# Optimization experiments

Hardware: AMD Instinct MI355X
Metric: run time of the kernel (lower is better)

Reference implementation:

```python
import jax, jax.numpy as jnp
import numpy as np
from jax import lax

EPS = 1e-5


def _conv3x3(inp, w):
    # NCHW input, OIHW kernel, VALID padding, stride 1 (matches nn.Conv2d(k=3, s=1, p=0))
    return lax.conv_general_dilated(inp, w, (1, 1), 'VALID',
                                    dimension_numbers=('NCHW', 'OIHW', 'NCHW'))


def _bn(h, gamma, beta, mean, var):
    # inference-mode BatchNorm2d
    inv = gamma / jnp.sqrt(var + EPS)
    return h * inv[None, :, None, None] + (beta - mean * inv)[None, :, None, None]


def _xcorr_depthwise(zf, xf):
    # per-sample, per-channel sliding cross-correlation: template zf over search xf
    B, C, Hz, Wz = zf.shape
    _, _, Hx, Wx = xf.shape
    xr = xf.reshape(1, B * C, Hx, Wx)
    kr = zf.reshape(B * C, 1, Hz, Wz)
    out = lax.conv_general_dilated(xr, kr, (1, 1), 'VALID',
                                   feature_group_count=B * C,
                                   dimension_numbers=('NCHW', 'OIHW', 'NCHW'))
    return out.reshape(B, C, out.shape[2], out.shape[3])


def setup_inputs() -> dict:
    key = jax.random.key(0)
    ks = jax.random.split(key, 12)
    B, Cin, Ch = 64, 256, 256
    z = jax.random.normal(ks[0], (B, Cin, 16, 16), dtype=jnp.float32)
    x = jax.random.normal(ks[1], (B, Cin, 32, 32), dtype=jnp.float32)
    # conv weights ~ N(0, 0.01) as in _initialize_weights
    w_z = 0.01 * jax.random.normal(ks[2], (Ch, Cin, 3, 3), dtype=jnp.float32)
    w_x = 0.01 * jax.random.normal(ks[3], (Ch, Cin, 3, 3), dtype=jnp.float32)
    gamma_z = 0.5 + jax.random.uniform(ks[4], (Ch,), dtype=jnp.float32)
    beta_z = 0.1 * jax.random.normal(ks[5], (Ch,), dtype=jnp.float32)
    mean_z = 0.1 * jax.random.normal(ks[6], (Ch,), dtype=jnp.float32)
    var_z = 0.5 + jax.random.uniform(ks[7], (Ch,), dtype=jnp.float32)
    gamma_x = 0.5 + jax.random.uniform(ks[8], (Ch,), dtype=jnp.float32)
    beta_x = 0.1 * jax.random.normal(ks[9], (Ch,), dtype=jnp.float32)
    mean_x = 0.1 * jax.random.normal(ks[10], (Ch,), dtype=jnp.float32)
    var_x = 0.5 + jax.random.uniform(ks[11], (Ch,), dtype=jnp.float32)
    return {'z': z, 'x': x, 'w_z': w_z, 'w_x': w_x,
            'gamma_z': gamma_z, 'beta_z': beta_z, 'mean_z': mean_z, 'var_z': var_z,
            'gamma_x': gamma_x, 'beta_x': beta_x, 'mean_x': mean_x, 'var_x': var_x}


def reference(z, x, w_z, w_x, gamma_z, beta_z, mean_z, var_z,
              gamma_x, beta_x, mean_x, var_x):
    zf = _bn(_conv3x3(z, w_z), gamma_z, beta_z, mean_z, var_z)   # [B,C,14,14]
    xf = _bn(_conv3x3(x, w_x), gamma_x, beta_x, mean_x, var_x)   # [B,C,30,30]
    return _xcorr_depthwise(zf, xf)                               # [B,C,17,17]
```

## Files before the change

kernel.cpp:

```cpp
#include <hip/hip_runtime.h>
#include <cstdint>
#include <cstddef>

typedef _Float16 f16;
typedef _Float16 half4 __attribute__((ext_vector_type(4)));
typedef _Float16 half8 __attribute__((ext_vector_type(8)));
typedef __fp16 fp16x2 __attribute__((ext_vector_type(2)));
typedef float f32x4 __attribute__((ext_vector_type(4)));

#define BN_EPS 1e-5f

#if defined(__has_builtin)
# if __has_builtin(__builtin_amdgcn_fdot2)
#  define HAVE_FDOT2 1
# endif
#endif
#ifndef HAVE_FDOT2
# define HAVE_FDOT2 0
#endif

static constexpr size_t OFF_XB  = 0;
static constexpr size_t OFF_ZB  = 33554432;
static constexpr size_t OFF_WX  = 41943040;
static constexpr size_t OFF_WZ  = 43122688;
static constexpr size_t OFF_BNX = 44302336;
static constexpr size_t OFF_BNZ = 44304384;
static constexpr size_t OFF_XFH = 44306432;
static constexpr size_t OFF_ZFH = 75763712;

__global__ __launch_bounds__(256) void prep_all(
    const float* __restrict__ x, const float* __restrict__ z,
    const float* __restrict__ w_x, const float* __restrict__ w_z,
    const float* __restrict__ gx, const float* __restrict__ bx,
    const float* __restrict__ mx, const float* __restrict__ vx,
    const float* __restrict__ gz, const float* __restrict__ bz,
    const float* __restrict__ mz, const float* __restrict__ vz,
    f16* __restrict__ xb, f16* __restrict__ zb,
    f16* __restrict__ wxA, f16* __restrict__ wzA,
    float* __restrict__ bnx, float* __restrict__ bnz) {
  __shared__ float tile[64][33];
  __shared__ alignas(16) f16 wtile[2304];
  const int bid = blockIdx.x;
  const int tid = threadIdx.x;
  if (bid < 12288) {
    const float* src; f16* dst; int lw, r;
    if (bid < 8192) { src = x; dst = xb; lw = 5; r = bid; }
    else            { src = z; dst = zb; lw = 4; r = bid - 8192; }
    const int W = 1 << lw;
    const int c0 = (r & 3) << 6;
    const int h = (r >> 2) & (W - 1);
    const int b = (r >> 2) >> lw;
    const float* sp = src + ((size_t)((b << 8) + c0) << (2 * lw)) + ((size_t)h << lw);
    const int w4 = W >> 2;
    const int n1 = w4 << 6;
    for (int i = tid; i < n1; i += 256) {
      int cl = i >> (lw - 2), c4 = i & (w4 - 1);
      float4 v = *(const float4*)(sp + ((size_t)cl << (2 * lw)) + (c4 << 2));
      int w0 = c4 << 2;
      tile[cl][w0] = v.x; tile[cl][w0 + 1] = v.y;
      tile[cl][w0 + 2] = v.z; tile[cl][w0 + 3] = v.w;
    }
    __syncthreads();
    f16* dp = dst + ((size_t)((b << lw) + h) << lw << 8) + c0;
    const int n2 = W << 3;
    for (int j = tid; j < n2; j += 256) {
      int w = j >> 3, cl0 = (j & 7) << 3;
      half8 o;
#pragma unroll
      for (int e = 0; e < 8; ++e) o[e] = (f16)tile[cl0 + e][w];
      *(half8*)(dp + (w << 8) + cl0) = o;
    }
  } else if (bid < 12800) {
    int r = bid - 12288;
    const float* src = (r < 256) ? w_x : w_z;
    f16* dst = (r < 256) ? wxA : wzA;
    int cout = r & 255;
    const float* sp = src + (size_t)cout * 2304;
    for (int i = tid; i < 2304; i += 256) {
      int cin = i / 9, khw = i - cin * 9;
      wtile[khw * 256 + cin] = (f16)sp[i];
    }
    __syncthreads();
    for (int c = tid; c < 288; c += 256) {
      int khw = c >> 5, cin0 = (c & 31) << 3;
      *(half8*)(dst + (khw << 16) + (cout << 8) + cin0) =
          *(const half8*)(wtile + khw * 256 + cin0);
    }
  } else {
    int c = tid;
    float iv = gx[c] / sqrtf(vx[c] + BN_EPS);
    bnx[c] = iv;
    bnx[256 + c] = bx[c] - mx[c] * iv;
    float iz = gz[c] / sqrtf(vz[c] + BN_EPS);
    bnz[c] = iz;
    bnz[256 + c] = bz[c] - mz[c] * iz;
  }
}

__device__ __forceinline__ void gl_lds16(const f16* g, f16* l) {
  __builtin_amdgcn_global_load_lds((__attribute__((address_space(1))) void*)g,
                                   (__attribute__((address_space(3))) void*)l, 16, 0, 0);
}

__global__ __launch_bounds__(256, 4) void conv_gemm_u(
    const f16* __restrict__ xb, const f16* __restrict__ zb,
    const f16* __restrict__ wx, const f16* __restrict__ wz,
    const float* __restrict__ bnx, const float* __restrict__ bnz,
    f16* __restrict__ xfh, f16* __restrict__ zfh) {
  __shared__ f16 As[128 * 64];
  __shared__ f16 Bs[128 * 64];
  const int g = blockIdx.x;
  const int pairIdx = ((g >> 4) << 3) | (g & 7);
  const int mblk = (g >> 3) & 1;
  if (pairIdx >= 548) return;
  const f16* inp; const f16* wA; const float* bn; f16* out;
  int nblk, HIN, WIN, WOUT, NPIX, WPAD, OPLANE;
  if (pairIdx < 450) {
    inp = xb; wA = wx; bn = bnx; out = xfh; nblk = pairIdx;
    HIN = 32; WIN = 32; WOUT = 30; NPIX = 900; WPAD = 32; OPLANE = 960;
  } else {
    inp = zb; wA = wz; bn = bnz; out = zfh; nblk = pairIdx - 450;
    HIN = 16; WIN = 16; WOUT = 14; NPIX = 196; WPAD = 16; OPLANE = 224;
  }
  const int tid = threadIdx.x;
  const int wid = tid >> 6, lane = tid & 63;
  const int wm = (wid >> 1) << 6, wn = (wid & 1) << 6;
  const int q = lane >> 4, lm = lane & 15;
  const int sr = lane >> 3, sc = lane & 7;
  const int swz = (sc ^ sr) << 3;
  const int mbase = mblk << 7;

  int arow[4], brow[4];
#pragma unroll
  for (int l = 0; l < 4; ++l) {
    int rr = (wid << 5) + (l << 3) + sr;
    arow[l] = ((mbase + rr) << 8) + swz;
    int n = (nblk << 7) + rr;
    int b = n / NPIX, rem = n - b * NPIX;
    int oh = rem / WOUT, ow = rem - oh * WOUT;
    brow[l] = (((b * HIN + oh) * WIN + ow) << 8) + swz;
  }

  f32x4 acc[4][4] = {};
  const int cA0 = (q ^ (lm & 7)) << 3;

  for (int kt = 0; kt < 36; ++kt) {
    const int cinb = kt / 9;
    const int khw = kt - cinb * 9;
    const int cin0 = cinb << 6;
    const int kh = khw / 3, kw = khw - kh * 3;
    const int wofs = (khw << 16) + cin0;
    const int iofs = ((kh * WIN + kw) << 8) + cin0;
#pragma unroll
    for (int l = 0; l < 4; ++l) {
      const int ldso = ((wid << 5) + (l << 3)) << 6;
      gl_lds16(wA + wofs + arow[l], As + ldso);
      gl_lds16(inp + iofs + brow[l], Bs + ldso);
    }
    __syncthreads();
#pragma unroll
    for (int h = 0; h < 2; ++h) {
      const int co = cA0 ^ (h << 5);
      half8 af[4], bf[4];
#pragma unroll
      for (int f = 0; f < 4; ++f) {
        af[f] = *(const half8*)&As[((wm + (f << 4) + lm) << 6) + co];
        bf[f] = *(const half8*)&Bs[((wn + (f << 4) + lm) << 6) + co];
      }
#pragma unroll
      for (int fm = 0; fm < 4; ++fm)
#pragma unroll
        for (int fn = 0; fn < 4; ++fn)
          acc[fm][fn] =
              __builtin_amdgcn_mfma_f32_16x16x32_f16(af[fm], bf[fn], acc[fm][fn], 0, 0, 0);
    }
    __syncthreads();
  }

#pragma unroll
  for (int fn = 0; fn < 4; ++fn) {
    int n_g = (nblk << 7) + wn + (fn << 4) + lm;
    int b = n_g / NPIX, rem = n_g - b * NPIX;
    int oh = rem / WOUT, ow = rem - oh * WOUT;
    f16* op = out + (size_t)(b << 8) * OPLANE + oh * WPAD + ow;
#pragma unroll
    for (int fm = 0; fm < 4; ++fm) {
      int m0 = mbase + wm + (fm << 4) + (q << 2);
#pragma unroll
      for (int rg = 0; rg < 4; ++rg) {
        int m = m0 + rg;
        op[(size_t)m * OPLANE] = (f16)(acc[fm][fn][rg] * bn[m] + bn[256 + m]);
      }
    }
  }
}

static constexpr int XST = 40;
static constexpr int XCH = 30 * XST;
static constexpr int ZCH = 14 * 16;

__global__ __launch_bounds__(256) void xcorr_dw3(const f16* __restrict__ zfh,
                                                 const f16* __restrict__ xfh,
                                                 float* __restrict__ out) {
  __shared__ f16 xs[3 * XCH];
  __shared__ f16 zs[3 * ZCH];
  const int t = threadIdx.x;
  const int ch0 = blockIdx.x * 3;

  for (int i = t; i < 360; i += 256) {
    int ch = i / 120, rem = i - ch * 120;
    int row = rem >> 2, col = (rem & 3) << 3;
    if (ch0 + ch < 16384)
      *(half8*)(xs + ch * XCH + row * XST + col) =
          *(const half8*)(xfh + (size_t)(ch0 + ch) * 960 + row * 32 + col);
  }
  for (int i = t; i < 84; i += 256) {
    int ch = i / 28, rem = i - ch * 28;
    if (ch0 + ch < 16384)
      *(half8*)(zs + ch * ZCH + rem * 8) =
          *(const half8*)(zfh + (size_t)(ch0 + ch) * 224 + rem * 8);
  }
  __syncthreads();

  int lc = t / 85;
  int r = t - lc * 85;
  const bool ok = (lc < 3) && (ch0 + lc < 16384);
  if (lc > 2) lc = 2;
  const int oy = r / 5, oxq = r - oy * 5, ox0 = oxq * 4;
  const f16* xbp = xs + lc * XCH;
  const f16* zbp = zs + lc * ZCH;

  float acc[4] = {0.f, 0.f, 0.f, 0.f};

#if HAVE_FDOT2
  union X20 { half4 v4[5]; fp16x2 h2[10]; };
  union Z16 { half8 v8[2]; fp16x2 h2[8]; };
#pragma unroll 2
  for (int u = 0; u < 14; ++u) {
    X20 xl;
#pragma unroll
    for (int k = 0; k < 5; ++k)
      xl.v4[k] = *(const half4*)(xbp + (oy + u) * XST + ox0 + (k << 2));
    Z16 zl;
    zl.v8[0] = *(const half8*)(zbp + u * 16);
    zl.v8[1] = *(const half8*)(zbp + u * 16 + 8);
    fp16x2 xo[8];
#pragma unroll
    for (int m = 0; m < 8; ++m) { xo[m][0] = xl.h2[m][1]; xo[m][1] = xl.h2[m + 1][0]; }
#pragma unroll
    for (int k = 0; k < 7; ++k) {
      acc[0] = __builtin_amdgcn_fdot2(zl.h2[k], xl.h2[k],     acc[0], false);
      acc[1] = __builtin_amdgcn_fdot2(zl.h2[k], xo[k],        acc[1], false);
      acc[2] = __builtin_amdgcn_fdot2(zl.h2[k], xl.h2[k + 1], acc[2], false);
      acc[3] = __builtin_amdgcn_fdot2(zl.h2[k], xo[k + 1],    acc[3], false);
    }
  }
#else
#pragma unroll 2
  for (int u = 0; u < 14; ++u) {
    float xr[20];
#pragma unroll
    for (int k = 0; k < 5; ++k) {
      half4 h = *(const half4*)(xbp + (oy + u) * XST + ox0 + k * 4);
#pragma unroll
      for (int e = 0; e < 4; ++e) xr[k * 4 + e] = (float)h[e];
    }
    float zc[14];
    {
      half8 z0 = *(const half8*)(zbp + u * 16);
      half8 z1 = *(const half8*)(zbp + u * 16 + 8);
#pragma unroll
      for (int e = 0; e < 8; ++e) zc[e] = (float)z0[e];
#pragma unroll
      for (int e = 0; e < 6; ++e) zc[8 + e] = (float)z1[e];
    }
#pragma unroll
    for (int v = 0; v < 14; ++v)
#pragma unroll
      for (int j = 0; j < 4; ++j) acc[j] = fmaf(zc[v], xr[v + j], acc[j]);
  }
#endif

  if (ok) {
    float* op = out + (size_t)(ch0 + lc) * 289 + oy * 17;
#pragma unroll
    for (int j = 0; j < 4; ++j) {
      int ox = ox0 + j;
      if (ox < 17) op[ox] = acc[j];
    }
  }
}

extern "C" void kernel_launch(void* const* d_in, const int* in_sizes, int n_in,
                              void* d_out, int out_size, void* d_ws, size_t ws_size,
                              hipStream_t stream) {
  const float* z = (const float*)d_in[0];
  const float* x = (const float*)d_in[1];
  const float* w_z = (const float*)d_in[2];
  const float* w_x = (const float*)d_in[3];
  const float* gamma_z = (const float*)d_in[4];
  const float* beta_z = (const float*)d_in[5];
  const float* mean_z = (const float*)d_in[6];
  const float* var_z = (const float*)d_in[7];
  const float* gamma_x = (const float*)d_in[8];
  const float* beta_x = (const float*)d_in[9];
  const float* mean_x = (const float*)d_in[10];
  const float* var_x = (const float*)d_in[11];

  char* ws = (char*)d_ws;
  f16* xb = (f16*)(ws + OFF_XB);
  f16* zb = (f16*)(ws + OFF_ZB);
  f16* wxA = (f16*)(ws + OFF_WX);
  f16* wzA = (f16*)(ws + OFF_WZ);
  float* bnx = (float*)(ws + OFF_BNX);
  float* bnz = (float*)(ws + OFF_BNZ);
  f16* xfh = (f16*)(ws + OFF_XFH);
  f16* zfh = (f16*)(ws + OFF_ZFH);
  float* out = (float*)d_out;

  prep_all<<<12801, 256, 0, stream>>>(x, z, w_x, w_z,
                                      gamma_x, beta_x, mean_x, var_x,
                                      gamma_z, beta_z, mean_z, var_z,
                                      xb, zb, wxA, wzA, bnx, bnz);

  conv_gemm_u<<<1104, 256, 0, stream>>>(xb, zb, wxA, wzA, bnx, bnz, xfh, zfh);

  xcorr_dw3<<<(16384 + 2) / 3, 256, 0, stream>>>(zfh, xfh, out);
}
```

Before: 285.9 us.

## Compute full output row per thread and pack 15 channels per block in xcorr

The depthwise xcorr kernel now gives each thread one entire 17-wide output row instead of a 4-wide strip, and each block handles 15 channels instead of 3. This cuts redundant LDS loads of overlapping x windows and the per-thread load and shuffle overhead per output, and it makes the grid smaller. In exchange each thread carries 17 accumulators plus 16 x pairs in registers, which may lower occupancy, LDS use per block grows, and 1 of 256 threads is idle.

```diff
diff --git a/kernel.cpp b/kernel.cpp
--- a/kernel.cpp
+++ b/kernel.cpp
@@ -195,75 +195,79 @@
   }
 }
 
-static constexpr int XST = 40;
-static constexpr int XCH = 30 * XST;
-static constexpr int ZCH = 14 * 16;
+static constexpr int XROWS = 30;
+static constexpr int XSTR  = 40;
+static constexpr int XCHN  = XROWS * XSTR;
+static constexpr int ZCHN  = 224;
+static constexpr int CPB   = 15;
 
 __global__ __launch_bounds__(256) void xcorr_dw3(const f16* __restrict__ zfh,
                                                  const f16* __restrict__ xfh,
                                                  float* __restrict__ out) {
-  __shared__ f16 xs[3 * XCH];
-  __shared__ f16 zs[3 * ZCH];
+  __shared__ alignas(16) f16 xs[CPB * XCHN];
+  __shared__ alignas(16) f16 zs[CPB * ZCHN];
   const int t = threadIdx.x;
-  const int ch0 = blockIdx.x * 3;
-
-  for (int i = t; i < 360; i += 256) {
+  const int ch0 = blockIdx.x * CPB;
+
+  for (int i = t; i < CPB * 30 * 4; i += 256) {
     int ch = i / 120, rem = i - ch * 120;
-    int row = rem >> 2, col = (rem & 3) << 3;
+    int row = rem >> 2, c8 = (rem & 3) << 3;
     if (ch0 + ch < 16384)
-      *(half8*)(xs + ch * XCH + row * XST + col) =
-          *(const half8*)(xfh + (size_t)(ch0 + ch) * 960 + row * 32 + col);
-  }
-  for (int i = t; i < 84; i += 256) {
+      *(half8*)(xs + ch * XCHN + row * XSTR + c8) =
+          *(const half8*)(xfh + (size_t)(ch0 + ch) * 960 + row * 32 + c8);
+  }
+  for (int i = t; i < CPB * 28; i += 256) {
     int ch = i / 28, rem = i - ch * 28;
     if (ch0 + ch < 16384)
-      *(half8*)(zs + ch * ZCH + rem * 8) =
+      *(half8*)(zs + ch * ZCHN + rem * 8) =
           *(const half8*)(zfh + (size_t)(ch0 + ch) * 224 + rem * 8);
   }
   __syncthreads();
 
-  int lc = t / 85;
-  int r = t - lc * 85;
-  const bool ok = (lc < 3) && (ch0 + lc < 16384);
-  if (lc > 2) lc = 2;
-  const int oy = r / 5, oxq = r - oy * 5, ox0 = oxq * 4;
-  const f16* xbp = xs + lc * XCH;
-  const f16* zbp = zs + lc * ZCH;
-
-  float acc[4] = {0.f, 0.f, 0.f, 0.f};
+  int lc = t / 17;
+  const int oy = t - lc * 17;
+  const bool ok = (lc < CPB) && (ch0 + lc < 16384);
+  if (lc >= CPB) lc = CPB - 1;
+  const f16* xbp = xs + lc * XCHN;
+  const f16* zbp = zs + lc * ZCHN;
+
+  float acc[17];
+#pragma unroll
+  for (int j = 0; j < 17; ++j) acc[j] = 0.f;
 
 #if HAVE_FDOT2
-  union X20 { half4 v4[5]; fp16x2 h2[10]; };
+  union X32 { half8 v8[4]; fp16x2 h2[16]; };
   union Z16 { half8 v8[2]; fp16x2 h2[8]; };
-#pragma unroll 2
   for (int u = 0; u < 14; ++u) {
-    X20 xl;
-#pragma unroll
-    for (int k = 0; k < 5; ++k)
-      xl.v4[k] = *(const half4*)(xbp + (oy + u) * XST + ox0 + (k << 2));
+    X32 xl;
+#pragma unroll
+    for (int k = 0; k < 4; ++k)
+      xl.v8[k] = *(const half8*)(xbp + (oy + u) * XSTR + (k << 3));
     Z16 zl;
     zl.v8[0] = *(const half8*)(zbp + u * 16);
     zl.v8[1] = *(const half8*)(zbp + u * 16 + 8);
-    fp16x2 xo[8];
-#pragma unroll
-    for (int m = 0; m < 8; ++m) { xo[m][0] = xl.h2[m][1]; xo[m][1] = xl.h2[m + 1][0]; }
-#pragma unroll
-    for (int k = 0; k < 7; ++k) {
-      acc[0] = __builtin_amdgcn_fdot2(zl.h2[k], xl.h2[k],     acc[0], false);
-      acc[1] = __builtin_amdgcn_fdot2(zl.h2[k], xo[k],        acc[1], false);
-      acc[2] = __builtin_amdgcn_fdot2(zl.h2[k], xl.h2[k + 1], acc[2], false);
-      acc[3] = __builtin_amdgcn_fdot2(zl.h2[k], xo[k + 1],    acc[3], false);
+    fp16x2 xo[15];
+#pragma unroll
+    for (int m = 0; m < 15; ++m) { xo[m][0] = xl.h2[m][1]; xo[m][1] = xl.h2[m + 1][0]; }
+#pragma unroll
+    for (int m = 0; m < 7; ++m) {
+#pragma unroll
+      for (int tt = 0; tt < 8; ++tt) {
+        acc[2 * tt]     = __builtin_amdgcn_fdot2(zl.h2[m], xl.h2[m + tt], acc[2 * tt], false);
+        acc[2 * tt + 1] = __builtin_amdgcn_fdot2(zl.h2[m], xo[m + tt],    acc[2 * tt + 1], false);
+      }
+      acc[16] = __builtin_amdgcn_fdot2(zl.h2[m], xl.h2[m + 8], acc[16], false);
     }
   }
 #else
-#pragma unroll 2
   for (int u = 0; u < 14; ++u) {
-    float xr[20];
-#pragma unroll
-    for (int k = 0; k < 5; ++k) {
-      half4 h = *(const half4*)(xbp + (oy + u) * XST + ox0 + k * 4);
-#pragma unroll
-      for (int e = 0; e < 4; ++e) xr[k * 4 + e] = (float)h[e];
+    float xr[30];
+#pragma unroll
+    for (int k = 0; k < 4; ++k) {
+      half8 h = *(const half8*)(xbp + (oy + u) * XSTR + (k << 3));
+#pragma unroll
+      for (int e = 0; e < 8; ++e)
+        if (k * 8 + e < 30) xr[k * 8 + e] = (float)h[e];
     }
     float zc[14];
     {
@@ -277,17 +281,14 @@
 #pragma unroll
     for (int v = 0; v < 14; ++v)
 #pragma unroll
-      for (int j = 0; j < 4; ++j) acc[j] = fmaf(zc[v], xr[v + j], acc[j]);
+      for (int j = 0; j < 17; ++j) acc[j] = fmaf(zc[v], xr[v + j], acc[j]);
   }
 #endif
 
   if (ok) {
     float* op = out + (size_t)(ch0 + lc) * 289 + oy * 17;
 #pragma unroll
-    for (int j = 0; j < 4; ++j) {
-      int ox = ox0 + j;
-      if (ox < 17) op[ox] = acc[j];
-    }
+    for (int j = 0; j < 17; ++j) op[j] = acc[j];
   }
 }
 
@@ -325,5 +326,5 @@
 
   conv_gemm_u<<<1104, 256, 0, stream>>>(xb, zb, wxA, wzA, bnx, bnz, xfh, zfh);
 
-  xcorr_dw3<<<(16384 + 2) / 3, 256, 0, stream>>>(zfh, xfh, out);
-}
+  xcorr_dw3<<<(16384 + CPB - 1) / CPB, 256, 0, stream>>>(zfh, xfh, out);
+}
```

Measured after the change: 276.0 us (median of 2 runs). -3.5%, faster.
